# Performance work log

Measured on AMD Instinct MI355X. Metric: run time of the kernel, lower is better.

## Reference

```python
import jax, jax.numpy as jnp
import numpy as np

THRESHOLD = 0.9
EPS = 1e-12


def setup_inputs() -> dict:
    key = jax.random.key(0)
    ks = jax.random.split(key, 7)
    B, D_in, H1, H2, D_out = 8192, 256, 512, 256, 64
    # torch Linear default init ~ U(-1/sqrt(fan_in), 1/sqrt(fan_in)); randn scaled is fine as a stand-in
    def lin(k, out_f, in_f):
        return jax.random.normal(k, (out_f, in_f), dtype=jnp.float32) / np.sqrt(in_f)
    return {
        "x": jax.random.normal(ks[0], (B, D_in), dtype=jnp.float32),
        "W1": lin(ks[1], H1, D_in),
        "b1": jax.random.normal(ks[2], (H1,), dtype=jnp.float32) * 0.01,
        "W2": lin(ks[3], H2, H1),
        "b2": jax.random.normal(ks[4], (H2,), dtype=jnp.float32) * 0.01,
        "W3": lin(ks[5], D_out, H2),
        "b3": jax.random.normal(ks[6], (D_out,), dtype=jnp.float32) * 0.01,
    }


def reference(x, W1, b1, W2, b2, W3, b3):
    # MLP: Linear -> Tanh -> Linear -> Tanh -> Linear (no tanh on last)
    h1 = jnp.tanh(x @ W1.T + b1)          # [B, 512]
    h2 = jnp.tanh(h1 @ W2.T + b2)         # [B, 256]
    out = h2 @ W3.T + b3                  # [B, 64]

    # Pairwise state fidelity: (normalized dot)^2, thresholded adjacency (diag excluded)
    norms = jnp.linalg.norm(out, axis=-1, keepdims=True)  # [B, 1]
    normed = out / (norms + EPS)
    fid = (normed @ normed.T) ** 2                         # [B, B]
    adj = (fid >= THRESHOLD).astype(out.dtype)
    B = out.shape[0]
    adj = adj * (1.0 - jnp.eye(B, dtype=out.dtype))        # no self-edges (i < j pairs only)

    return adj @ out                                       # [B, 64]
```

## Files before the change

### kernel.cpp

```cpp
#include <hip/hip_runtime.h>
#include <hip/hip_bf16.h>
#include <math.h>

#define B_ROWS 8192
#define D_IN   256
#define H1_DIM 512
#define H2_DIM 256
#define D_OUT  64
#define EPSF   1e-12f
#define THRESH 0.9f
#define GUARD 0.94f

typedef __attribute__((ext_vector_type(8))) short short8;
typedef __attribute__((ext_vector_type(4))) float f32x4;

__device__ inline void pack8(const float* __restrict__ src, short* __restrict__ dh,
                             short* __restrict__ dm, int t, int C, int lgq) {
  const int lane = t & 63;
  const int g = t >> 6;
  const int q = g & ((1 << lgq) - 1);
  const int I = g >> lgq;
  const int row = I * 16 + (lane & 15);
  const int k0 = q * 32 + ((lane >> 4) << 3);
  const float* p = src + (size_t)row * C + k0;
  float4 a = *(const float4*)p;
  float4 b = *(const float4*)(p + 4);
  float v[8] = {a.x, a.y, a.z, a.w, b.x, b.y, b.z, b.w};
  short h8[8], m8[8];
#pragma unroll
  for (int e = 0; e < 8; ++e) {
    __hip_bfloat16 h = __float2bfloat16(v[e]);
    float hf = __bfloat162float(h);
    __hip_bfloat16 m = __float2bfloat16(v[e] - hf);
    h8[e] = *(short*)&h;
    m8[e] = *(short*)&m;
  }
  *(short8*)(dh + (size_t)t * 8) = *(short8*)h8;
  *(short8*)(dm + (size_t)t * 8) = *(short8*)m8;
}

__global__ __launch_bounds__(256)
void pack_inputs(const float* __restrict__ x, const float* __restrict__ W1,
                 const float* __restrict__ W2, const float* __restrict__ W3,
                 short* xh, short* xm, short* w1h, short* w1m,
                 short* w2h, short* w2m, short* w3h, short* w3m) {
  const int b = blockIdx.x;
  const int tid = threadIdx.x;
  if (b < 1024)       pack8(x,  xh,  xm,  b * 256 + tid, 256, 3);
  else if (b < 1088)  pack8(W1, w1h, w1m, (b - 1024) * 256 + tid, 256, 3);
  else if (b < 1152)  pack8(W2, w2h, w2m, (b - 1088) * 256 + tid, 512, 4);
  else                pack8(W3, w3h, w3m, (b - 1152) * 256 + tid, 256, 3);
}

template<int KSTEPS, int JT, int MODE>
__global__ __launch_bounds__(256, 2)
void mfma_gemm(const short* __restrict__ pAh, const short* __restrict__ pAm,
               const short* __restrict__ pBh, const short* __restrict__ pBm,
               const float* __restrict__ bias, float* __restrict__ Cout,
               short* __restrict__ dh, short* __restrict__ dm, int N,
               float* __restrict__ rz, float* __restrict__ invng) {
  constexpr int ITB = 4;
  constexpr int BTJ = 2 * JT;
  constexpr int NITEMS = 2 * ITB + 2 * BTJ;
  constexpr int PER_WAVE = NITEMS / 4;
  constexpr int WCOL = 16 * JT + 4;
  union SM {
    struct {
      short Ah[2][ITB * 512];
      short Am[2][ITB * 512];
      short Bh[2][BTJ * 512];
      short Bm[2][BTJ * 512];
    } st;
    float wbuf[4 * 32 * WCOL];
  };
  __shared__ __align__(16) SM sm;
  __shared__ float nsum[2][64];
  __shared__ float invn[64];

  const int tid = threadIdx.x;
  const int wave = tid >> 6, lane = tid & 63;
  const int wi = wave >> 1, wj = wave & 1;
  const int bIt0 = blockIdx.x * ITB;
  const int bJt0 = blockIdx.y * BTJ;

  if constexpr (MODE == 2) {
    float4* rz4 = (float4*)(rz + (size_t)blockIdx.x * 64 * 64);
#pragma unroll
    for (int u = 0; u < 4; ++u)
      rz4[u * 256 + tid] = make_float4(0.f, 0.f, 0.f, 0.f);
  }

  f32x4 acc[2][JT];
#pragma unroll
  for (int a = 0; a < 2; ++a)
#pragma unroll
    for (int b = 0; b < JT; ++b) acc[a][b] = (f32x4){0.f, 0.f, 0.f, 0.f};

  auto stage = [&](int q, int bf) {
#pragma unroll
    for (int u = 0; u < PER_WAVE; ++u) {
      const int item = wave * PER_WAVE + u;
      const short* src;
      short* dst;
      if (item < 2 * ITB) {
        const int t = item >> 1;
        const int m = item & 1;
        src = (m ? pAm : pAh) + ((size_t)(bIt0 + t) * KSTEPS + q) * 512;
        dst = (m ? sm.st.Am : sm.st.Ah)[bf] + t * 512;
      } else {
        const int e = item - 2 * ITB;
        const int t = e >> 1;
        const int m = e & 1;
        src = (m ? pBm : pBh) + ((size_t)(bJt0 + t) * KSTEPS + q) * 512;
        dst = (m ? sm.st.Bm : sm.st.Bh)[bf] + t * 512;
      }
      __builtin_amdgcn_global_load_lds(
          (const __attribute__((address_space(1))) void*)(src + lane * 8),
          (__attribute__((address_space(3))) void*)dst, 16, 0, 0);
    }
  };

  stage(0, 0);
  for (int q = 0; q < KSTEPS; ++q) {
    __syncthreads();
    if (q + 1 < KSTEPS) stage(q + 1, (q + 1) & 1);
    const int bf = q & 1;
    short8 Ah[2], Am[2];
#pragma unroll
    for (int it = 0; it < 2; ++it) {
      Ah[it] = *(const short8*)(sm.st.Ah[bf] + (wi * 2 + it) * 512 + lane * 8);
      Am[it] = *(const short8*)(sm.st.Am[bf] + (wi * 2 + it) * 512 + lane * 8);
    }
    short8 Bh[JT], Bm[JT];
#pragma unroll
    for (int jt = 0; jt < JT; ++jt) {
      Bh[jt] = *(const short8*)(sm.st.Bh[bf] + (wj * JT + jt) * 512 + lane * 8);
      Bm[jt] = *(const short8*)(sm.st.Bm[bf] + (wj * JT + jt) * 512 + lane * 8);
    }
#pragma unroll
    for (int it = 0; it < 2; ++it)
#pragma unroll
      for (int jt = 0; jt < JT; ++jt) {
        acc[it][jt] = __builtin_amdgcn_mfma_f32_16x16x32_bf16(Ah[it], Bh[jt], acc[it][jt], 0, 0, 0);
        acc[it][jt] = __builtin_amdgcn_mfma_f32_16x16x32_bf16(Ah[it], Bm[jt], acc[it][jt], 0, 0, 0);
        acc[it][jt] = __builtin_amdgcn_mfma_f32_16x16x32_bf16(Am[it], Bh[jt], acc[it][jt], 0, 0, 0);
      }
  }
  __syncthreads();

  float bv[JT];
#pragma unroll
  for (int jt = 0; jt < JT; ++jt)
    bv[jt] = bias[(bJt0 + wj * JT + jt) * 16 + (lane & 15)];

  if constexpr (MODE == 1) {
#pragma unroll
    for (int it = 0; it < 2; ++it)
#pragma unroll
      for (int jt = 0; jt < JT; ++jt)
#pragma unroll
        for (int r = 0; r < 4; ++r) {
          const float val = tanhf(acc[it][jt][r] + bv[jt]);
          const int row_l = it * 16 + (lane >> 4) * 4 + r;
          const int col_l = jt * 16 + (lane & 15);
          sm.wbuf[(wave * 32 + row_l) * WCOL + col_l] = val;
        }
    __syncthreads();
  } else {
#pragma unroll
    for (int it = 0; it < 2; ++it)
#pragma unroll
      for (int r = 0; r < 4; ++r) {
        float sq = 0.f;
        const int row_l = it * 16 + (lane >> 4) * 4 + r;
#pragma unroll
        for (int jt = 0; jt < JT; ++jt) {
          const float val = acc[it][jt][r] + bv[jt];
          const int col_l = jt * 16 + (lane & 15);
          sm.wbuf[(wave * 32 + row_l) * WCOL + col_l] = val;
          const int row = (bIt0 + wi * 2 + it) * 16 + (lane >> 4) * 4 + r;
          Cout[(size_t)row * N + wj * (16 * JT) + col_l] = val;
          sq = fmaf(val, val, sq);
        }
#pragma unroll
        for (int m = 1; m < 16; m <<= 1) sq += __shfl_xor(sq, m, 64);
        if ((lane & 15) == 0) nsum[wj][wi * 32 + row_l] = sq;
      }
    __syncthreads();
    if (tid < 64) {
      const float iv = 1.0f / (sqrtf(nsum[0][tid] + nsum[1][tid]) + EPSF);
      invn[tid] = iv;
      invng[blockIdx.x * 64 + tid] = iv;
    }
    __syncthreads();
  }

  constexpr int QLMAX = (JT >= 2) ? (JT / 2) : 1;
#pragma unroll
  for (int itl = 0; itl < 2; ++itl)
#pragma unroll
    for (int ql = 0; ql < QLMAX; ++ql) {
      const int row_l = itl * 16 + (lane & 15);
      const int kl = ql * 32 + ((lane >> 4) << 3);
      const float* wp = &sm.wbuf[(wave * 32 + row_l) * WCOL + kl];
      const float scale = (MODE == 2) ? invn[wi * 32 + row_l] : 1.0f;
      float4 a = *(const float4*)wp;
      float4 b = *(const float4*)(wp + 4);
      float v[8] = {a.x, a.y, a.z, a.w, b.x, b.y, b.z, b.w};
      short h8[8], m8[8];
#pragma unroll
      for (int e = 0; e < 8; ++e) {
        const float sv = v[e] * scale;
        __hip_bfloat16 h = __float2bfloat16(sv);
        h8[e] = *(short*)&h;
        if constexpr (MODE == 1) {
          float hf = __bfloat162float(h);
          __hip_bfloat16 m = __float2bfloat16(sv - hf);
          m8[e] = *(short*)&m;
        }
      }
      const int ItG = bIt0 + wi * 2 + itl;
      const int qG = (((bJt0 + wj * JT) * 16) + ql * 32) >> 5;
      const size_t off = ((size_t)(ItG * (N >> 5) + qG) * 64 + lane) * 8;
      *(short8*)(dh + off) = *(short8*)h8;
      if constexpr (MODE == 1) *(short8*)(dm + off) = *(short8*)m8;
    }
}

#define JSPLIT 8
#define CT 8
#define NCHUNK (B_ROWS / JSPLIT / 16 / CT)

__global__ __launch_bounds__(256, 2)
void gram_accum(const short* __restrict__ vph, const float* __restrict__ out,
                const float* __restrict__ invn, float* __restrict__ res) {
  __shared__ __align__(16) short lh[2][CT * 1024];
  const int tid = threadIdx.x;
  const int wave = tid >> 6;
  const int lane = tid & 63;
  const int i0 = blockIdx.x * 128;
  const int jbase = blockIdx.y * (B_ROWS / JSPLIT);

  short8 Ah[8][2];
#pragma unroll
  for (int it = 0; it < 8; ++it) {
    const int It = (i0 >> 4) + it;
#pragma unroll
    for (int q = 0; q < 2; ++q)
      Ah[it][q] = *(const short8*)(vph + (size_t)It * 1024 + q * 512 + lane * 8);
  }

  auto stage = [&](int c, int bf) {
    const size_t base = ((size_t)(jbase >> 4) + c * CT) * 1024;
#pragma unroll
    for (int u = 0; u < 4; ++u) {
      const int item = wave * 4 + u;
      const short* src = vph + base + item * 512;
      short* dst = lh[bf] + item * 512;
      __builtin_amdgcn_global_load_lds(
          (const __attribute__((address_space(1))) void*)(src + lane * 8),
          (__attribute__((address_space(3))) void*)dst, 16, 0, 0);
    }
  };

  stage(0, 0);
  for (int c = 0; c < NCHUNK; ++c) {
    __syncthreads();
    if (c + 1 < NCHUNK) stage(c + 1, (c + 1) & 1);
    const int bf = c & 1;
#pragma unroll
    for (int t = 0; t < 2; ++t) {
      const int jt = wave * 2 + t;
      const int j0 = jbase + (c * CT + jt) * 16;
      short8 Bh0 = *(const short8*)(lh[bf] + jt * 1024 + lane * 8);
      short8 Bh1 = *(const short8*)(lh[bf] + jt * 1024 + 512 + lane * 8);
      f32x4 g[8];
#pragma unroll
      for (int it = 0; it < 8; ++it) g[it] = (f32x4){0.f, 0.f, 0.f, 0.f};
#pragma unroll
      for (int it = 0; it < 8; ++it) g[it] = __builtin_amdgcn_mfma_f32_16x16x32_bf16(Ah[it][0], Bh0, g[it], 0, 0, 0);
#pragma unroll
      for (int it = 0; it < 8; ++it) g[it] = __builtin_amdgcn_mfma_f32_16x16x32_bf16(Ah[it][1], Bh1, g[it], 0, 0, 0);
#pragma unroll
      for (int it = 0; it < 8; ++it) {
        const float m01 = fmaxf(fabsf(g[it][0]), fabsf(g[it][1]));
        const float m23 = fmaxf(fabsf(g[it][2]), fabsf(g[it][3]));
        if (fmaxf(m01, m23) >= GUARD) {
          const int j = j0 + (lane & 15);
          const float ivj = invn[j];
          const float* __restrict__ oj = out + (size_t)j * D_OUT;
#pragma unroll
          for (int r = 0; r < 4; ++r) {
            if (fabsf(g[it][r]) >= GUARD) {
              const int i = i0 + it * 16 + (lane >> 4) * 4 + r;
              if (i != j) {
                const float* __restrict__ oi = out + (size_t)i * D_OUT;
                float d = 0.f;
                for (int k = 0; k < D_OUT; k += 4) {
                  float4 a = *(const float4*)(oi + k);
                  float4 b = *(const float4*)(oj + k);
                  d = fmaf(a.x, b.x, d); d = fmaf(a.y, b.y, d);
                  d = fmaf(a.z, b.z, d); d = fmaf(a.w, b.w, d);
                }
                const float nd = d * invn[i] * ivj;
                if (nd * nd >= THRESH) {
                  float* __restrict__ ri = res + (size_t)i * D_OUT;
                  for (int k = 0; k < D_OUT; ++k) atomicAdd(&ri[k], oj[k]);
                }
              }
            }
          }
        }
      }
    }
  }
}

#define MB (1024 * 1024)

extern "C" void kernel_launch(void* const* d_in, const int* in_sizes, int n_in,
                              void* d_out, int out_size, void* d_ws, size_t ws_size,
                              hipStream_t stream) {
  const float* x  = (const float*)d_in[0];
  const float* W1 = (const float*)d_in[1];
  const float* b1 = (const float*)d_in[2];
  const float* W2 = (const float*)d_in[3];
  const float* b2 = (const float*)d_in[4];
  const float* W3 = (const float*)d_in[5];
  const float* b3 = (const float*)d_in[6];
  float* res = (float*)d_out;

  char* ws = (char*)d_ws;
  short* xh  = (short*)(ws + 0 * MB);
  short* xm  = (short*)(ws + 4 * MB);
  short* h2h = (short*)(ws + 0 * MB);
  short* h2m = (short*)(ws + 4 * MB);
  short* h1h = (short*)(ws + 8 * MB);
  short* h1m = (short*)(ws + 16 * MB);
  float* out  = (float*)(ws + 8 * MB);
  short* vph  = (short*)(ws + 11 * MB);
  float* invn = (float*)(ws + 12 * MB);
  short* w1h = (short*)(ws + 24 * MB);
  short* w1m = (short*)(ws + 24 * MB + 256 * 1024);
  short* w2h = (short*)(ws + 24 * MB + 512 * 1024);
  short* w2m = (short*)(ws + 24 * MB + 768 * 1024);
  short* w3h = (short*)(ws + 25 * MB);
  short* w3m = (short*)(ws + 25 * MB + 32 * 1024);

  pack_inputs<<<1160, 256, 0, stream>>>(x, W1, W2, W3, xh, xm, w1h, w1m, w2h, w2m, w3h, w3m);
  mfma_gemm<8, 4, 1><<<dim3(128, 4), 256, 0, stream>>>(
      xh, xm, w1h, w1m, b1, nullptr, h1h, h1m, H1_DIM, nullptr, nullptr);
  mfma_gemm<16, 2, 1><<<dim3(128, 4), 256, 0, stream>>>(
      h1h, h1m, w2h, w2m, b2, nullptr, h2h, h2m, H2_DIM, nullptr, nullptr);
  mfma_gemm<8, 2, 2><<<dim3(128, 1), 256, 0, stream>>>(
      h2h, h2m, w3h, w3m, b3, out, vph, nullptr, D_OUT, res, invn);
  gram_accum<<<dim3(B_ROWS / 128, JSPLIT), 256, 0, stream>>>(vph, out, invn, res);
}
```

Before: 127.2 us.

## Fuse three MLP GEMM layers into one kernel keeping activations on-chip

Replaces the x-packing kernel and three separate split-bf16 MFMA GEMM launches with one fused kernel. Each block handles 64 rows, converts x to hi/lo bf16 in registers, and streams W1/W2 chunks through LDS so the h1 and h2 activations never reach global memory. This removes the global round trips for the intermediate activations and two launches. In exchange the grid is only 128 blocks with one block per CU, heavy register use (acc2[16] plus A operands), and many serialized barriers per chunk, so occupancy and latency hiding may suffer.

```diff
diff --git a/kernel.cpp b/kernel.cpp
--- a/kernel.cpp
+++ b/kernel.cpp
@@ -40,191 +40,257 @@
 }
 
 __global__ __launch_bounds__(256)
-void pack_inputs(const float* __restrict__ x, const float* __restrict__ W1,
-                 const float* __restrict__ W2, const float* __restrict__ W3,
-                 short* xh, short* xm, short* w1h, short* w1m,
-                 short* w2h, short* w2m, short* w3h, short* w3m) {
+void pack_weights(const float* __restrict__ W1, const float* __restrict__ W2,
+                  const float* __restrict__ W3,
+                  short* w1h, short* w1m, short* w2h, short* w2m,
+                  short* w3h, short* w3m) {
   const int b = blockIdx.x;
   const int tid = threadIdx.x;
-  if (b < 1024)       pack8(x,  xh,  xm,  b * 256 + tid, 256, 3);
-  else if (b < 1088)  pack8(W1, w1h, w1m, (b - 1024) * 256 + tid, 256, 3);
-  else if (b < 1152)  pack8(W2, w2h, w2m, (b - 1088) * 256 + tid, 512, 4);
-  else                pack8(W3, w3h, w3m, (b - 1152) * 256 + tid, 256, 3);
+  if (b < 64)       pack8(W1, w1h, w1m, b * 256 + tid, 256, 3);
+  else if (b < 128) pack8(W2, w2h, w2m, (b - 64) * 256 + tid, 512, 4);
+  else              pack8(W3, w3h, w3m, (b - 128) * 256 + tid, 256, 3);
 }
 
-template<int KSTEPS, int JT, int MODE>
-__global__ __launch_bounds__(256, 2)
-void mfma_gemm(const short* __restrict__ pAh, const short* __restrict__ pAm,
-               const short* __restrict__ pBh, const short* __restrict__ pBm,
-               const float* __restrict__ bias, float* __restrict__ Cout,
-               short* __restrict__ dh, short* __restrict__ dm, int N,
-               float* __restrict__ rz, float* __restrict__ invng) {
-  constexpr int ITB = 4;
-  constexpr int BTJ = 2 * JT;
-  constexpr int NITEMS = 2 * ITB + 2 * BTJ;
-  constexpr int PER_WAVE = NITEMS / 4;
-  constexpr int WCOL = 16 * JT + 4;
-  union SM {
-    struct {
-      short Ah[2][ITB * 512];
-      short Am[2][ITB * 512];
-      short Bh[2][BTJ * 512];
-      short Bm[2][BTJ * 512];
-    } st;
-    float wbuf[4 * 32 * WCOL];
-  };
-  __shared__ __align__(16) SM sm;
-  __shared__ float nsum[2][64];
-  __shared__ float invn[64];
+__global__ __launch_bounds__(256, 1)
+void fused_mlp(const float* __restrict__ x,
+               const short* __restrict__ w1h, const short* __restrict__ w1m,
+               const short* __restrict__ w2h, const short* __restrict__ w2m,
+               const short* __restrict__ w3h, const short* __restrict__ w3m,
+               const float* __restrict__ b1, const float* __restrict__ b2,
+               const float* __restrict__ b3,
+               float* __restrict__ out, short* __restrict__ vph,
+               float* __restrict__ invng, float* __restrict__ res) {
+  __shared__ __align__(16) short w1s[2 * 2 * 8 * 512];
+  __shared__ __align__(16) short w2s[2 * 16 * 512];
+  __shared__ __align__(16) float tb[4][16][36];
+  __shared__ float invb[64];
 
   const int tid = threadIdx.x;
   const int wave = tid >> 6, lane = tid & 63;
-  const int wi = wave >> 1, wj = wave & 1;
-  const int bIt0 = blockIdx.x * ITB;
-  const int bJt0 = blockIdx.y * BTJ;
-
-  if constexpr (MODE == 2) {
-    float4* rz4 = (float4*)(rz + (size_t)blockIdx.x * 64 * 64);
-#pragma unroll
-    for (int u = 0; u < 4; ++u)
-      rz4[u * 256 + tid] = make_float4(0.f, 0.f, 0.f, 0.f);
-  }
-
-  f32x4 acc[2][JT];
-#pragma unroll
-  for (int a = 0; a < 2; ++a)
-#pragma unroll
-    for (int b = 0; b < JT; ++b) acc[a][b] = (f32x4){0.f, 0.f, 0.f, 0.f};
-
-  auto stage = [&](int q, int bf) {
-#pragma unroll
-    for (int u = 0; u < PER_WAVE; ++u) {
-      const int item = wave * PER_WAVE + u;
-      const short* src;
-      short* dst;
-      if (item < 2 * ITB) {
-        const int t = item >> 1;
-        const int m = item & 1;
-        src = (m ? pAm : pAh) + ((size_t)(bIt0 + t) * KSTEPS + q) * 512;
-        dst = (m ? sm.st.Am : sm.st.Ah)[bf] + t * 512;
-      } else {
-        const int e = item - 2 * ITB;
-        const int t = e >> 1;
-        const int m = e & 1;
-        src = (m ? pBm : pBh) + ((size_t)(bJt0 + t) * KSTEPS + q) * 512;
-        dst = (m ? sm.st.Bm : sm.st.Bh)[bf] + t * 512;
+  const int rr = lane & 15, gg = lane >> 4;
+  const int R0 = blockIdx.x * 64 + wave * 16;
+
+  {
+    float4* rz = (float4*)(res + (size_t)blockIdx.x * 64 * 64);
+#pragma unroll
+    for (int u = 0; u < 4; ++u) rz[u * 256 + tid] = make_float4(0.f, 0.f, 0.f, 0.f);
+  }
+
+  short8 A1h[8], A1m[8];
+#pragma unroll
+  for (int q = 0; q < 8; ++q) {
+    const float* p = x + (size_t)(R0 + rr) * D_IN + q * 32 + gg * 8;
+    float4 a = *(const float4*)p;
+    float4 b = *(const float4*)(p + 4);
+    float v[8] = {a.x, a.y, a.z, a.w, b.x, b.y, b.z, b.w};
+    short h8[8], m8[8];
+#pragma unroll
+    for (int e = 0; e < 8; ++e) {
+      __hip_bfloat16 h = __float2bfloat16(v[e]);
+      float hf = __bfloat162float(h);
+      __hip_bfloat16 m = __float2bfloat16(v[e] - hf);
+      h8[e] = *(short*)&h;
+      m8[e] = *(short*)&m;
+    }
+    A1h[q] = *(short8*)h8;
+    A1m[q] = *(short8*)m8;
+  }
+
+  auto stage_w1 = [&](int c) {
+#pragma unroll
+    for (int u = 0; u < 8; ++u) {
+      const int item = wave * 8 + u;
+      const int m = item >> 4, t = (item >> 3) & 1, q = item & 7;
+      const short* src = (m ? w1m : w1h) + ((size_t)((2 * c + t) * 8 + q)) * 512 + lane * 8;
+      __builtin_amdgcn_global_load_lds(
+          (const __attribute__((address_space(1))) void*)src,
+          (__attribute__((address_space(3))) void*)(w1s + item * 512), 16, 0, 0);
+    }
+  };
+  auto stage_w2 = [&](int c) {
+#pragma unroll
+    for (int u = 0; u < 8; ++u) {
+      const int item = wave * 8 + u;
+      const int m = item >> 4, jt = item & 15;
+      const short* src = (m ? w2m : w2h) + ((size_t)(jt * 16 + c)) * 512 + lane * 8;
+      __builtin_amdgcn_global_load_lds(
+          (const __attribute__((address_space(1))) void*)src,
+          (__attribute__((address_space(3))) void*)(w2s + item * 512), 16, 0, 0);
+    }
+  };
+
+  f32x4 acc2[16];
+#pragma unroll
+  for (int j = 0; j < 16; ++j) acc2[j] = (f32x4){0.f, 0.f, 0.f, 0.f};
+
+  stage_w1(0);
+  stage_w2(0);
+  __syncthreads();
+
+#pragma unroll 1
+  for (int c = 0; c < 16; ++c) {
+    float hv[2][4];
+#pragma unroll
+    for (int jt = 0; jt < 2; ++jt) {
+      f32x4 g = {0.f, 0.f, 0.f, 0.f};
+#pragma unroll
+      for (int q = 0; q < 8; ++q) {
+        short8 Bh = *(const short8*)(w1s + ((jt * 8 + q) << 9) + lane * 8);
+        short8 Bm = *(const short8*)(w1s + (((2 + jt) * 8 + q) << 9) + lane * 8);
+        g = __builtin_amdgcn_mfma_f32_16x16x32_bf16(A1h[q], Bh, g, 0, 0, 0);
+        g = __builtin_amdgcn_mfma_f32_16x16x32_bf16(A1h[q], Bm, g, 0, 0, 0);
+        g = __builtin_amdgcn_mfma_f32_16x16x32_bf16(A1m[q], Bh, g, 0, 0, 0);
       }
-      __builtin_amdgcn_global_load_lds(
-          (const __attribute__((address_space(1))) void*)(src + lane * 8),
-          (__attribute__((address_space(3))) void*)dst, 16, 0, 0);
-    }
-  };
-
-  stage(0, 0);
-  for (int q = 0; q < KSTEPS; ++q) {
-    __syncthreads();
-    if (q + 1 < KSTEPS) stage(q + 1, (q + 1) & 1);
-    const int bf = q & 1;
-    short8 Ah[2], Am[2];
-#pragma unroll
-    for (int it = 0; it < 2; ++it) {
-      Ah[it] = *(const short8*)(sm.st.Ah[bf] + (wi * 2 + it) * 512 + lane * 8);
-      Am[it] = *(const short8*)(sm.st.Am[bf] + (wi * 2 + it) * 512 + lane * 8);
-    }
-    short8 Bh[JT], Bm[JT];
-#pragma unroll
-    for (int jt = 0; jt < JT; ++jt) {
-      Bh[jt] = *(const short8*)(sm.st.Bh[bf] + (wj * JT + jt) * 512 + lane * 8);
-      Bm[jt] = *(const short8*)(sm.st.Bm[bf] + (wj * JT + jt) * 512 + lane * 8);
-    }
-#pragma unroll
-    for (int it = 0; it < 2; ++it)
-#pragma unroll
-      for (int jt = 0; jt < JT; ++jt) {
-        acc[it][jt] = __builtin_amdgcn_mfma_f32_16x16x32_bf16(Ah[it], Bh[jt], acc[it][jt], 0, 0, 0);
-        acc[it][jt] = __builtin_amdgcn_mfma_f32_16x16x32_bf16(Ah[it], Bm[jt], acc[it][jt], 0, 0, 0);
-        acc[it][jt] = __builtin_amdgcn_mfma_f32_16x16x32_bf16(Am[it], Bh[jt], acc[it][jt], 0, 0, 0);
-      }
-  }
-  __syncthreads();
-
-  float bv[JT];
-#pragma unroll
-  for (int jt = 0; jt < JT; ++jt)
-    bv[jt] = bias[(bJt0 + wj * JT + jt) * 16 + (lane & 15)];
-
-  if constexpr (MODE == 1) {
-#pragma unroll
-    for (int it = 0; it < 2; ++it)
-#pragma unroll
-      for (int jt = 0; jt < JT; ++jt)
-#pragma unroll
-        for (int r = 0; r < 4; ++r) {
-          const float val = tanhf(acc[it][jt][r] + bv[jt]);
-          const int row_l = it * 16 + (lane >> 4) * 4 + r;
-          const int col_l = jt * 16 + (lane & 15);
-          sm.wbuf[(wave * 32 + row_l) * WCOL + col_l] = val;
-        }
-    __syncthreads();
-  } else {
-#pragma unroll
-    for (int it = 0; it < 2; ++it)
-#pragma unroll
-      for (int r = 0; r < 4; ++r) {
-        float sq = 0.f;
-        const int row_l = it * 16 + (lane >> 4) * 4 + r;
-#pragma unroll
-        for (int jt = 0; jt < JT; ++jt) {
-          const float val = acc[it][jt][r] + bv[jt];
-          const int col_l = jt * 16 + (lane & 15);
-          sm.wbuf[(wave * 32 + row_l) * WCOL + col_l] = val;
-          const int row = (bIt0 + wi * 2 + it) * 16 + (lane >> 4) * 4 + r;
-          Cout[(size_t)row * N + wj * (16 * JT) + col_l] = val;
-          sq = fmaf(val, val, sq);
-        }
-#pragma unroll
-        for (int m = 1; m < 16; m <<= 1) sq += __shfl_xor(sq, m, 64);
-        if ((lane & 15) == 0) nsum[wj][wi * 32 + row_l] = sq;
-      }
-    __syncthreads();
-    if (tid < 64) {
-      const float iv = 1.0f / (sqrtf(nsum[0][tid] + nsum[1][tid]) + EPSF);
-      invn[tid] = iv;
-      invng[blockIdx.x * 64 + tid] = iv;
-    }
-    __syncthreads();
-  }
-
-  constexpr int QLMAX = (JT >= 2) ? (JT / 2) : 1;
-#pragma unroll
-  for (int itl = 0; itl < 2; ++itl)
-#pragma unroll
-    for (int ql = 0; ql < QLMAX; ++ql) {
-      const int row_l = itl * 16 + (lane & 15);
-      const int kl = ql * 32 + ((lane >> 4) << 3);
-      const float* wp = &sm.wbuf[(wave * 32 + row_l) * WCOL + kl];
-      const float scale = (MODE == 2) ? invn[wi * 32 + row_l] : 1.0f;
-      float4 a = *(const float4*)wp;
-      float4 b = *(const float4*)(wp + 4);
+      const float bv = b1[(2 * c + jt) * 16 + rr];
+#pragma unroll
+      for (int r = 0; r < 4; ++r) hv[jt][r] = tanhf(g[r] + bv);
+    }
+#pragma unroll
+    for (int jt = 0; jt < 2; ++jt)
+#pragma unroll
+      for (int r = 0; r < 4; ++r)
+        tb[wave][gg * 4 + r][jt * 16 + rr] = hv[jt][r];
+    __syncthreads();
+    if (c + 1 < 16) stage_w1(c + 1);
+
+    short8 A2h, A2m;
+    {
+      const float* tp = &tb[wave][rr][gg * 8];
+      float4 a = *(const float4*)tp;
+      float4 b = *(const float4*)(tp + 4);
       float v[8] = {a.x, a.y, a.z, a.w, b.x, b.y, b.z, b.w};
       short h8[8], m8[8];
 #pragma unroll
       for (int e = 0; e < 8; ++e) {
-        const float sv = v[e] * scale;
-        __hip_bfloat16 h = __float2bfloat16(sv);
+        __hip_bfloat16 h = __float2bfloat16(v[e]);
+        float hf = __bfloat162float(h);
+        __hip_bfloat16 m = __float2bfloat16(v[e] - hf);
         h8[e] = *(short*)&h;
-        if constexpr (MODE == 1) {
-          float hf = __bfloat162float(h);
-          __hip_bfloat16 m = __float2bfloat16(sv - hf);
-          m8[e] = *(short*)&m;
-        }
+        m8[e] = *(short*)&m;
       }
-      const int ItG = bIt0 + wi * 2 + itl;
-      const int qG = (((bJt0 + wj * JT) * 16) + ql * 32) >> 5;
-      const size_t off = ((size_t)(ItG * (N >> 5) + qG) * 64 + lane) * 8;
-      *(short8*)(dh + off) = *(short8*)h8;
-      if constexpr (MODE == 1) *(short8*)(dm + off) = *(short8*)m8;
-    }
+      A2h = *(short8*)h8;
+      A2m = *(short8*)m8;
+    }
+#pragma unroll
+    for (int jt2 = 0; jt2 < 16; ++jt2) {
+      short8 Bh = *(const short8*)(w2s + (jt2 << 9) + lane * 8);
+      short8 Bm = *(const short8*)(w2s + ((16 + jt2) << 9) + lane * 8);
+      acc2[jt2] = __builtin_amdgcn_mfma_f32_16x16x32_bf16(A2h, Bh, acc2[jt2], 0, 0, 0);
+      acc2[jt2] = __builtin_amdgcn_mfma_f32_16x16x32_bf16(A2h, Bm, acc2[jt2], 0, 0, 0);
+      acc2[jt2] = __builtin_amdgcn_mfma_f32_16x16x32_bf16(A2m, Bh, acc2[jt2], 0, 0, 0);
+    }
+    __syncthreads();
+    if (c + 1 < 16) stage_w2(c + 1);
+  }
+
+#pragma unroll
+  for (int u = 0; u < 16; ++u) {
+    const int item = wave * 16 + u;
+    const int m = item >> 5, rest = item & 31;
+    const short* src = (m ? w3m : w3h) + ((size_t)rest) * 512 + lane * 8;
+    short* dst = (item < 32) ? (w1s + item * 512) : (w2s + (item - 32) * 512);
+    __builtin_amdgcn_global_load_lds(
+        (const __attribute__((address_space(1))) void*)src,
+        (__attribute__((address_space(3))) void*)dst, 16, 0, 0);
+  }
+
+  short8 A3h[8], A3m[8];
+#pragma unroll
+  for (int q3 = 0; q3 < 8; ++q3) {
+#pragma unroll
+    for (int jt = 0; jt < 2; ++jt) {
+      const int jt2 = q3 * 2 + jt;
+      const float bv = b2[jt2 * 16 + rr];
+#pragma unroll
+      for (int r = 0; r < 4; ++r)
+        tb[wave][gg * 4 + r][jt * 16 + rr] = tanhf(acc2[jt2][r] + bv);
+    }
+    __syncthreads();
+    {
+      const float* tp = &tb[wave][rr][gg * 8];
+      float4 a = *(const float4*)tp;
+      float4 b = *(const float4*)(tp + 4);
+      float v[8] = {a.x, a.y, a.z, a.w, b.x, b.y, b.z, b.w};
+      short h8[8], m8[8];
+#pragma unroll
+      for (int e = 0; e < 8; ++e) {
+        __hip_bfloat16 h = __float2bfloat16(v[e]);
+        float hf = __bfloat162float(h);
+        __hip_bfloat16 m = __float2bfloat16(v[e] - hf);
+        h8[e] = *(short*)&h;
+        m8[e] = *(short*)&m;
+      }
+      A3h[q3] = *(short8*)h8;
+      A3m[q3] = *(short8*)m8;
+    }
+    __syncthreads();
+  }
+
+  f32x4 acc3[4];
+#pragma unroll
+  for (int t = 0; t < 4; ++t) acc3[t] = (f32x4){0.f, 0.f, 0.f, 0.f};
+#pragma unroll
+  for (int q3 = 0; q3 < 8; ++q3)
+#pragma unroll
+    for (int t = 0; t < 4; ++t) {
+      short8 Bh = *(const short8*)(w1s + ((t * 8 + q3) << 9) + lane * 8);
+      short8 Bm = *(const short8*)(w2s + ((t * 8 + q3) << 9) + lane * 8);
+      acc3[t] = __builtin_amdgcn_mfma_f32_16x16x32_bf16(A3h[q3], Bh, acc3[t], 0, 0, 0);
+      acc3[t] = __builtin_amdgcn_mfma_f32_16x16x32_bf16(A3h[q3], Bm, acc3[t], 0, 0, 0);
+      acc3[t] = __builtin_amdgcn_mfma_f32_16x16x32_bf16(A3m[q3], Bh, acc3[t], 0, 0, 0);
+    }
+
+  float val[4][4];
+#pragma unroll
+  for (int t = 0; t < 4; ++t) {
+    const float bv = b3[t * 16 + rr];
+#pragma unroll
+    for (int r = 0; r < 4; ++r) val[t][r] = acc3[t][r] + bv;
+  }
+#pragma unroll
+  for (int t = 0; t < 4; ++t)
+#pragma unroll
+    for (int r = 0; r < 4; ++r)
+      out[(size_t)(R0 + gg * 4 + r) * D_OUT + t * 16 + rr] = val[t][r];
+#pragma unroll
+  for (int r = 0; r < 4; ++r) {
+    float sq = 0.f;
+#pragma unroll
+    for (int t = 0; t < 4; ++t) sq = fmaf(val[t][r], val[t][r], sq);
+#pragma unroll
+    for (int m = 1; m < 16; m <<= 1) sq += __shfl_xor(sq, m, 64);
+    if (rr == 0) {
+      const float iv = 1.0f / (sqrtf(sq) + EPSF);
+      invb[wave * 16 + gg * 4 + r] = iv;
+      invng[R0 + gg * 4 + r] = iv;
+    }
+  }
+  __syncthreads();
+  const int ItG = blockIdx.x * 4 + wave;
+#pragma unroll
+  for (int q = 0; q < 2; ++q) {
+#pragma unroll
+    for (int jt = 0; jt < 2; ++jt)
+#pragma unroll
+      for (int r = 0; r < 4; ++r)
+        tb[wave][gg * 4 + r][jt * 16 + rr] = val[2 * q + jt][r];
+    __syncthreads();
+    {
+      const float* tp = &tb[wave][rr][gg * 8];
+      float4 a = *(const float4*)tp;
+      float4 b = *(const float4*)(tp + 4);
+      const float sc = invb[wave * 16 + rr];
+      float v[8] = {a.x, a.y, a.z, a.w, b.x, b.y, b.z, b.w};
+      short h8[8];
+#pragma unroll
+      for (int e = 0; e < 8; ++e) {
+        __hip_bfloat16 h = __float2bfloat16(v[e] * sc);
+        h8[e] = *(short*)&h;
+      }
+      *(short8*)(vph + ((size_t)(ItG * 2 + q) * 64 + lane) * 8) = *(short8*)h8;
+    }
+    __syncthreads();
+  }
 }
 
 #define JSPLIT 8
@@ -331,12 +397,6 @@
   float* res = (float*)d_out;
 
   char* ws = (char*)d_ws;
-  short* xh  = (short*)(ws + 0 * MB);
-  short* xm  = (short*)(ws + 4 * MB);
-  short* h2h = (short*)(ws + 0 * MB);
-  short* h2m = (short*)(ws + 4 * MB);
-  short* h1h = (short*)(ws + 8 * MB);
-  short* h1m = (short*)(ws + 16 * MB);
   float* out  = (float*)(ws + 8 * MB);
   short* vph  = (short*)(ws + 11 * MB);
   float* invn = (float*)(ws + 12 * MB);
@@ -347,12 +407,8 @@
   short* w3h = (short*)(ws + 25 * MB);
   short* w3m = (short*)(ws + 25 * MB + 32 * 1024);
 
-  pack_inputs<<<1160, 256, 0, stream>>>(x, W1, W2, W3, xh, xm, w1h, w1m, w2h, w2m, w3h, w3m);
-  mfma_gemm<8, 4, 1><<<dim3(128, 4), 256, 0, stream>>>(
-      xh, xm, w1h, w1m, b1, nullptr, h1h, h1m, H1_DIM, nullptr, nullptr);
-  mfma_gemm<16, 2, 1><<<dim3(128, 4), 256, 0, stream>>>(
-      h1h, h1m, w2h, w2m, b2, nullptr, h2h, h2m, H2_DIM, nullptr, nullptr);
-  mfma_gemm<8, 2, 2><<<dim3(128, 1), 256, 0, stream>>>(
-      h2h, h2m, w3h, w3m, b3, out, vph, nullptr, D_OUT, res, invn);
+  pack_weights<<<136, 256, 0, stream>>>(W1, W2, W3, w1h, w1m, w2h, w2m, w3h, w3m);
+  fused_mlp<<<B_ROWS / 64, 256, 0, stream>>>(
+      x, w1h, w1m, w2h, w2m, w3h, w3m, b1, b2, b3, out, vph, invn, res);
   gram_accum<<<dim3(B_ROWS / 128, JSPLIT), 256, 0, stream>>>(vph, out, invn, res);
 }
```

Measured after the change: 145.8 us. +14.7%, slower.

## Fuse fp32-to-bf16 split packing of inputs and weights into GEMM load stages

Applied to the files above, without the earlier changes.

Removes the separate pack_inputs kernel. The GEMMs now load raw fp32 x and weight tiles into registers, split each value into bf16 high and low parts, and write both into shared memory inside the double-buffered K loop. This saves one kernel launch and the write and re-read of the packed buffers. In exchange, weight tiles are re-converted by every block, adding ALU work and register pressure inside the main loop.

```diff
diff --git a/kernel.cpp b/kernel.cpp
--- a/kernel.cpp
+++ b/kernel.cpp
@@ -14,55 +14,18 @@
 typedef __attribute__((ext_vector_type(8))) short short8;
 typedef __attribute__((ext_vector_type(4))) float f32x4;
 
-__device__ inline void pack8(const float* __restrict__ src, short* __restrict__ dh,
-                             short* __restrict__ dm, int t, int C, int lgq) {
-  const int lane = t & 63;
-  const int g = t >> 6;
-  const int q = g & ((1 << lgq) - 1);
-  const int I = g >> lgq;
-  const int row = I * 16 + (lane & 15);
-  const int k0 = q * 32 + ((lane >> 4) << 3);
-  const float* p = src + (size_t)row * C + k0;
-  float4 a = *(const float4*)p;
-  float4 b = *(const float4*)(p + 4);
-  float v[8] = {a.x, a.y, a.z, a.w, b.x, b.y, b.z, b.w};
-  short h8[8], m8[8];
-#pragma unroll
-  for (int e = 0; e < 8; ++e) {
-    __hip_bfloat16 h = __float2bfloat16(v[e]);
-    float hf = __bfloat162float(h);
-    __hip_bfloat16 m = __float2bfloat16(v[e] - hf);
-    h8[e] = *(short*)&h;
-    m8[e] = *(short*)&m;
-  }
-  *(short8*)(dh + (size_t)t * 8) = *(short8*)h8;
-  *(short8*)(dm + (size_t)t * 8) = *(short8*)m8;
-}
-
-__global__ __launch_bounds__(256)
-void pack_inputs(const float* __restrict__ x, const float* __restrict__ W1,
-                 const float* __restrict__ W2, const float* __restrict__ W3,
-                 short* xh, short* xm, short* w1h, short* w1m,
-                 short* w2h, short* w2m, short* w3h, short* w3m) {
-  const int b = blockIdx.x;
-  const int tid = threadIdx.x;
-  if (b < 1024)       pack8(x,  xh,  xm,  b * 256 + tid, 256, 3);
-  else if (b < 1088)  pack8(W1, w1h, w1m, (b - 1024) * 256 + tid, 256, 3);
-  else if (b < 1152)  pack8(W2, w2h, w2m, (b - 1088) * 256 + tid, 512, 4);
-  else                pack8(W3, w3h, w3m, (b - 1152) * 256 + tid, 256, 3);
-}
-
-template<int KSTEPS, int JT, int MODE>
+template<int KSTEPS, int JT, int MODE, bool ARAW>
 __global__ __launch_bounds__(256, 2)
-void mfma_gemm(const short* __restrict__ pAh, const short* __restrict__ pAm,
-               const short* __restrict__ pBh, const short* __restrict__ pBm,
+void mfma_gemm(const float* __restrict__ Araw,
+               const short* __restrict__ pAh, const short* __restrict__ pAm,
+               const float* __restrict__ Braw,
                const float* __restrict__ bias, float* __restrict__ Cout,
                short* __restrict__ dh, short* __restrict__ dm, int N,
                float* __restrict__ rz, float* __restrict__ invng) {
+  constexpr int K = KSTEPS * 32;
   constexpr int ITB = 4;
   constexpr int BTJ = 2 * JT;
-  constexpr int NITEMS = 2 * ITB + 2 * BTJ;
-  constexpr int PER_WAVE = NITEMS / 4;
+  constexpr int BPW = JT / 2;
   constexpr int WCOL = 16 * JT + 4;
   union SM {
     struct {
@@ -75,11 +38,12 @@
   };
   __shared__ __align__(16) SM sm;
   __shared__ float nsum[2][64];
-  __shared__ float invn[64];
+  __shared__ float invb[64];
 
   const int tid = threadIdx.x;
   const int wave = tid >> 6, lane = tid & 63;
   const int wi = wave >> 1, wj = wave & 1;
+  const int rr = lane & 15, gg = lane >> 4;
   const int bIt0 = blockIdx.x * ITB;
   const int bJt0 = blockIdx.y * BTJ;
 
@@ -90,41 +54,76 @@
       rz4[u * 256 + tid] = make_float4(0.f, 0.f, 0.f, 0.f);
   }
 
-  f32x4 acc[2][JT];
-#pragma unroll
-  for (int a = 0; a < 2; ++a)
-#pragma unroll
-    for (int b = 0; b < JT; ++b) acc[a][b] = (f32x4){0.f, 0.f, 0.f, 0.f};
-
-  auto stage = [&](int q, int bf) {
-#pragma unroll
-    for (int u = 0; u < PER_WAVE; ++u) {
-      const int item = wave * PER_WAVE + u;
-      const short* src;
-      short* dst;
-      if (item < 2 * ITB) {
-        const int t = item >> 1;
-        const int m = item & 1;
-        src = (m ? pAm : pAh) + ((size_t)(bIt0 + t) * KSTEPS + q) * 512;
-        dst = (m ? sm.st.Am : sm.st.Ah)[bf] + t * 512;
-      } else {
-        const int e = item - 2 * ITB;
-        const int t = e >> 1;
-        const int m = e & 1;
-        src = (m ? pBm : pBh) + ((size_t)(bJt0 + t) * KSTEPS + q) * 512;
-        dst = (m ? sm.st.Bm : sm.st.Bh)[bf] + t * 512;
-      }
+  float ar[8];
+  float br[BPW][8];
+
+  auto gload8 = [&](const float* __restrict__ p, float* r) {
+    float4 a = *(const float4*)p;
+    float4 b = *(const float4*)(p + 4);
+    r[0] = a.x; r[1] = a.y; r[2] = a.z; r[3] = a.w;
+    r[4] = b.x; r[5] = b.y; r[6] = b.z; r[7] = b.w;
+  };
+
+  auto loads = [&](int q) {
+    if constexpr (ARAW)
+      gload8(Araw + (size_t)((bIt0 + wave) * 16 + rr) * K + q * 32 + gg * 8, ar);
+#pragma unroll
+    for (int u = 0; u < BPW; ++u)
+      gload8(Braw + (size_t)((bJt0 + wave * BPW + u) * 16 + rr) * K + q * 32 + gg * 8, br[u]);
+  };
+
+  auto stageA = [&](int q, int bf) {
+#pragma unroll
+    for (int u = 0; u < 2; ++u) {
+      const int item = wave * 2 + u;
+      const int t = item >> 1, m = item & 1;
+      const short* src = (m ? pAm : pAh) + ((size_t)(bIt0 + t) * KSTEPS + q) * 512;
+      short* dst = (m ? sm.st.Am : sm.st.Ah)[bf] + t * 512;
       __builtin_amdgcn_global_load_lds(
           (const __attribute__((address_space(1))) void*)(src + lane * 8),
           (__attribute__((address_space(3))) void*)dst, 16, 0, 0);
     }
   };
 
-  stage(0, 0);
+  auto split_write = [&](const float* r, short* dsth, short* dstm) {
+    short h8[8], m8[8];
+#pragma unroll
+    for (int e = 0; e < 8; ++e) {
+      __hip_bfloat16 h = __float2bfloat16(r[e]);
+      float hf = __bfloat162float(h);
+      __hip_bfloat16 m = __float2bfloat16(r[e] - hf);
+      h8[e] = *(short*)&h;
+      m8[e] = *(short*)&m;
+    }
+    *(short8*)(dsth + lane * 8) = *(short8*)h8;
+    *(short8*)(dstm + lane * 8) = *(short8*)m8;
+  };
+
+  auto cvt_write = [&](int bf) {
+    if constexpr (ARAW)
+      split_write(ar, sm.st.Ah[bf] + wave * 512, sm.st.Am[bf] + wave * 512);
+#pragma unroll
+    for (int u = 0; u < BPW; ++u)
+      split_write(br[u], sm.st.Bh[bf] + (wave * BPW + u) * 512,
+                         sm.st.Bm[bf] + (wave * BPW + u) * 512);
+  };
+
+  f32x4 acc[2][JT];
+#pragma unroll
+  for (int a = 0; a < 2; ++a)
+#pragma unroll
+    for (int b = 0; b < JT; ++b) acc[a][b] = (f32x4){0.f, 0.f, 0.f, 0.f};
+
+  loads(0);
+  if constexpr (!ARAW) stageA(0, 0);
+  cvt_write(0);
   for (int q = 0; q < KSTEPS; ++q) {
     __syncthreads();
-    if (q + 1 < KSTEPS) stage(q + 1, (q + 1) & 1);
-    const int bf = q & 1;
+    const int bf = q & 1, nbf = (q + 1) & 1;
+    if (q + 1 < KSTEPS) {
+      loads(q + 1);
+      if constexpr (!ARAW) stageA(q + 1, nbf);
+    }
     short8 Ah[2], Am[2];
 #pragma unroll
     for (int it = 0; it < 2; ++it) {
@@ -145,13 +144,14 @@
         acc[it][jt] = __builtin_amdgcn_mfma_f32_16x16x32_bf16(Ah[it], Bm[jt], acc[it][jt], 0, 0, 0);
         acc[it][jt] = __builtin_amdgcn_mfma_f32_16x16x32_bf16(Am[it], Bh[jt], acc[it][jt], 0, 0, 0);
       }
+    if (q + 1 < KSTEPS) cvt_write(nbf);
   }
   __syncthreads();
 
   float bv[JT];
 #pragma unroll
   for (int jt = 0; jt < JT; ++jt)
-    bv[jt] = bias[(bJt0 + wj * JT + jt) * 16 + (lane & 15)];
+    bv[jt] = bias[(bJt0 + wj * JT + jt) * 16 + rr];
 
   if constexpr (MODE == 1) {
 #pragma unroll
@@ -161,8 +161,8 @@
 #pragma unroll
         for (int r = 0; r < 4; ++r) {
           const float val = tanhf(acc[it][jt][r] + bv[jt]);
-          const int row_l = it * 16 + (lane >> 4) * 4 + r;
-          const int col_l = jt * 16 + (lane & 15);
+          const int row_l = it * 16 + gg * 4 + r;
+          const int col_l = jt * 16 + rr;
           sm.wbuf[(wave * 32 + row_l) * WCOL + col_l] = val;
         }
     __syncthreads();
@@ -172,24 +172,24 @@
 #pragma unroll
       for (int r = 0; r < 4; ++r) {
         float sq = 0.f;
-        const int row_l = it * 16 + (lane >> 4) * 4 + r;
+        const int row_l = it * 16 + gg * 4 + r;
 #pragma unroll
         for (int jt = 0; jt < JT; ++jt) {
           const float val = acc[it][jt][r] + bv[jt];
-          const int col_l = jt * 16 + (lane & 15);
+          const int col_l = jt * 16 + rr;
           sm.wbuf[(wave * 32 + row_l) * WCOL + col_l] = val;
-          const int row = (bIt0 + wi * 2 + it) * 16 + (lane >> 4) * 4 + r;
+          const int row = (bIt0 + wi * 2 + it) * 16 + gg * 4 + r;
           Cout[(size_t)row * N + wj * (16 * JT) + col_l] = val;
           sq = fmaf(val, val, sq);
         }
 #pragma unroll
         for (int m = 1; m < 16; m <<= 1) sq += __shfl_xor(sq, m, 64);
-        if ((lane & 15) == 0) nsum[wj][wi * 32 + row_l] = sq;
+        if (rr == 0) nsum[wj][wi * 32 + row_l] = sq;
       }
     __syncthreads();
     if (tid < 64) {
       const float iv = 1.0f / (sqrtf(nsum[0][tid] + nsum[1][tid]) + EPSF);
-      invn[tid] = iv;
+      invb[tid] = iv;
       invng[blockIdx.x * 64 + tid] = iv;
     }
     __syncthreads();
@@ -200,10 +200,10 @@
   for (int itl = 0; itl < 2; ++itl)
 #pragma unroll
     for (int ql = 0; ql < QLMAX; ++ql) {
-      const int row_l = itl * 16 + (lane & 15);
-      const int kl = ql * 32 + ((lane >> 4) << 3);
+      const int row_l = itl * 16 + rr;
+      const int kl = ql * 32 + gg * 8;
       const float* wp = &sm.wbuf[(wave * 32 + row_l) * WCOL + kl];
-      const float scale = (MODE == 2) ? invn[wi * 32 + row_l] : 1.0f;
+      const float scale = (MODE == 2) ? invb[wi * 32 + row_l] : 1.0f;
       float4 a = *(const float4*)wp;
       float4 b = *(const float4*)(wp + 4);
       float v[8] = {a.x, a.y, a.z, a.w, b.x, b.y, b.z, b.w};
@@ -331,8 +331,6 @@
   float* res = (float*)d_out;
 
   char* ws = (char*)d_ws;
-  short* xh  = (short*)(ws + 0 * MB);
-  short* xm  = (short*)(ws + 4 * MB);
   short* h2h = (short*)(ws + 0 * MB);
   short* h2m = (short*)(ws + 4 * MB);
   short* h1h = (short*)(ws + 8 * MB);
@@ -340,19 +338,12 @@
   float* out  = (float*)(ws + 8 * MB);
   short* vph  = (short*)(ws + 11 * MB);
   float* invn = (float*)(ws + 12 * MB);
-  short* w1h = (short*)(ws + 24 * MB);
-  short* w1m = (short*)(ws + 24 * MB + 256 * 1024);
-  short* w2h = (short*)(ws + 24 * MB + 512 * 1024);
-  short* w2m = (short*)(ws + 24 * MB + 768 * 1024);
-  short* w3h = (short*)(ws + 25 * MB);
-  short* w3m = (short*)(ws + 25 * MB + 32 * 1024);
-
-  pack_inputs<<<1160, 256, 0, stream>>>(x, W1, W2, W3, xh, xm, w1h, w1m, w2h, w2m, w3h, w3m);
-  mfma_gemm<8, 4, 1><<<dim3(128, 4), 256, 0, stream>>>(
-      xh, xm, w1h, w1m, b1, nullptr, h1h, h1m, H1_DIM, nullptr, nullptr);
-  mfma_gemm<16, 2, 1><<<dim3(128, 4), 256, 0, stream>>>(
-      h1h, h1m, w2h, w2m, b2, nullptr, h2h, h2m, H2_DIM, nullptr, nullptr);
-  mfma_gemm<8, 2, 2><<<dim3(128, 1), 256, 0, stream>>>(
-      h2h, h2m, w3h, w3m, b3, out, vph, nullptr, D_OUT, res, invn);
+
+  mfma_gemm<8, 4, 1, true><<<dim3(128, 4), 256, 0, stream>>>(
+      x, nullptr, nullptr, W1, b1, nullptr, h1h, h1m, H1_DIM, nullptr, nullptr);
+  mfma_gemm<16, 2, 1, false><<<dim3(128, 4), 256, 0, stream>>>(
+      nullptr, h1h, h1m, W2, b2, nullptr, h2h, h2m, H2_DIM, nullptr, nullptr);
+  mfma_gemm<8, 2, 2, false><<<dim3(128, 1), 256, 0, stream>>>(
+      nullptr, h2h, h2m, W3, b3, out, vph, nullptr, D_OUT, res, invn);
   gram_accum<<<dim3(B_ROWS / 128, JSPLIT), 256, 0, stream>>>(vph, out, invn, res);
 }
```

Result: slower. 139.9 us (+10.0%).

## Fuse x bf16 hi/lo split into first GEMM, holding A fragments in registers

Applied to the files above, without the earlier changes.

The separate packing pass over x is dropped. The first GEMM now loads raw fp32 x tiles into padded shared memory, splits them into bf16 hi/lo fragments, and keeps all K-step A fragments in registers for the whole loop. This removes the write and re-read of the packed x buffers (about 8 MB of traffic) and shrinks the pack kernel to weights only. In exchange it raises register pressure (32 short8 values per thread) and shared-memory use, and each of the 4 column blocks recomputes the split for the same x rows.

```diff
diff --git a/kernel.cpp b/kernel.cpp
--- a/kernel.cpp
+++ b/kernel.cpp
@@ -40,34 +40,36 @@
 }
 
 __global__ __launch_bounds__(256)
-void pack_inputs(const float* __restrict__ x, const float* __restrict__ W1,
-                 const float* __restrict__ W2, const float* __restrict__ W3,
-                 short* xh, short* xm, short* w1h, short* w1m,
-                 short* w2h, short* w2m, short* w3h, short* w3m) {
+void pack_weights(const float* __restrict__ W1, const float* __restrict__ W2,
+                  const float* __restrict__ W3,
+                  short* w1h, short* w1m, short* w2h, short* w2m,
+                  short* w3h, short* w3m) {
   const int b = blockIdx.x;
   const int tid = threadIdx.x;
-  if (b < 1024)       pack8(x,  xh,  xm,  b * 256 + tid, 256, 3);
-  else if (b < 1088)  pack8(W1, w1h, w1m, (b - 1024) * 256 + tid, 256, 3);
-  else if (b < 1152)  pack8(W2, w2h, w2m, (b - 1088) * 256 + tid, 512, 4);
-  else                pack8(W3, w3h, w3m, (b - 1152) * 256 + tid, 256, 3);
+  if (b < 64)       pack8(W1, w1h, w1m, b * 256 + tid, 256, 3);
+  else if (b < 128) pack8(W2, w2h, w2m, (b - 64) * 256 + tid, 512, 4);
+  else              pack8(W3, w3h, w3m, (b - 128) * 256 + tid, 256, 3);
 }
 
-template<int KSTEPS, int JT, int MODE>
+template<int KSTEPS, int JT, int MODE, bool AXREG>
 __global__ __launch_bounds__(256, 2)
-void mfma_gemm(const short* __restrict__ pAh, const short* __restrict__ pAm,
+void mfma_gemm(const float* __restrict__ Araw,
+               const short* __restrict__ pAh, const short* __restrict__ pAm,
                const short* __restrict__ pBh, const short* __restrict__ pBm,
                const float* __restrict__ bias, float* __restrict__ Cout,
                short* __restrict__ dh, short* __restrict__ dm, int N,
                float* __restrict__ rz, float* __restrict__ invng) {
   constexpr int ITB = 4;
   constexpr int BTJ = 2 * JT;
-  constexpr int NITEMS = 2 * ITB + 2 * BTJ;
+  constexpr int NITEMS = (AXREG ? 0 : 2 * ITB) + 2 * BTJ;
   constexpr int PER_WAVE = NITEMS / 4;
   constexpr int WCOL = 16 * JT + 4;
+  constexpr int XP = 257;
   union SM {
+    float xs[AXREG ? 64 * XP : 1];
     struct {
-      short Ah[2][ITB * 512];
-      short Am[2][ITB * 512];
+      short Ah[2][(AXREG ? 1 : ITB) * 512];
+      short Am[2][(AXREG ? 1 : ITB) * 512];
       short Bh[2][BTJ * 512];
       short Bm[2][BTJ * 512];
     } st;
@@ -75,11 +77,12 @@
   };
   __shared__ __align__(16) SM sm;
   __shared__ float nsum[2][64];
-  __shared__ float invn[64];
+  __shared__ float invb[64];
 
   const int tid = threadIdx.x;
   const int wave = tid >> 6, lane = tid & 63;
   const int wi = wave >> 1, wj = wave & 1;
+  const int rr = lane & 15, gg = lane >> 4;
   const int bIt0 = blockIdx.x * ITB;
   const int bJt0 = blockIdx.y * BTJ;
 
@@ -90,11 +93,42 @@
       rz4[u * 256 + tid] = make_float4(0.f, 0.f, 0.f, 0.f);
   }
 
-  f32x4 acc[2][JT];
-#pragma unroll
-  for (int a = 0; a < 2; ++a)
-#pragma unroll
-    for (int b = 0; b < JT; ++b) acc[a][b] = (f32x4){0.f, 0.f, 0.f, 0.f};
+  short8 Axh[AXREG ? 2 : 1][AXREG ? KSTEPS : 1];
+  short8 Axm[AXREG ? 2 : 1][AXREG ? KSTEPS : 1];
+  if constexpr (AXREG) {
+    constexpr int K = KSTEPS * 32;
+#pragma unroll
+    for (int u = 0; u < 16; ++u) {
+      const int f = u * 256 + tid;
+      const int row = f >> 6, c4 = f & 63;
+      *(float4*)&sm.xs[row * XP + c4 * 4] =
+          *(const float4*)(Araw + (size_t)(bIt0 * 16 + row) * K + c4 * 4);
+    }
+    __syncthreads();
+#pragma unroll
+    for (int it = 0; it < 2; ++it) {
+      const int row = (wi * 2 + it) * 16 + rr;
+#pragma unroll
+      for (int q = 0; q < KSTEPS; ++q) {
+        const float* p = &sm.xs[row * XP + q * 32 + gg * 8];
+        float4 a = *(const float4*)p;
+        float4 b = *(const float4*)(p + 4);
+        float v[8] = {a.x, a.y, a.z, a.w, b.x, b.y, b.z, b.w};
+        short h8[8], m8[8];
+#pragma unroll
+        for (int e = 0; e < 8; ++e) {
+          __hip_bfloat16 h = __float2bfloat16(v[e]);
+          float hf = __bfloat162float(h);
+          __hip_bfloat16 m = __float2bfloat16(v[e] - hf);
+          h8[e] = *(short*)&h;
+          m8[e] = *(short*)&m;
+        }
+        Axh[it][q] = *(short8*)h8;
+        Axm[it][q] = *(short8*)m8;
+      }
+    }
+    __syncthreads();
+  }
 
   auto stage = [&](int q, int bf) {
 #pragma unroll
@@ -102,13 +136,13 @@
       const int item = wave * PER_WAVE + u;
       const short* src;
       short* dst;
-      if (item < 2 * ITB) {
+      if (!AXREG && item < 2 * ITB) {
         const int t = item >> 1;
         const int m = item & 1;
         src = (m ? pAm : pAh) + ((size_t)(bIt0 + t) * KSTEPS + q) * 512;
         dst = (m ? sm.st.Am : sm.st.Ah)[bf] + t * 512;
       } else {
-        const int e = item - 2 * ITB;
+        const int e = item - (AXREG ? 0 : 2 * ITB);
         const int t = e >> 1;
         const int m = e & 1;
         src = (m ? pBm : pBh) + ((size_t)(bJt0 + t) * KSTEPS + q) * 512;
@@ -120,7 +154,14 @@
     }
   };
 
+  f32x4 acc[2][JT];
+#pragma unroll
+  for (int a = 0; a < 2; ++a)
+#pragma unroll
+    for (int b = 0; b < JT; ++b) acc[a][b] = (f32x4){0.f, 0.f, 0.f, 0.f};
+
   stage(0, 0);
+#pragma unroll
   for (int q = 0; q < KSTEPS; ++q) {
     __syncthreads();
     if (q + 1 < KSTEPS) stage(q + 1, (q + 1) & 1);
@@ -128,8 +169,13 @@
     short8 Ah[2], Am[2];
 #pragma unroll
     for (int it = 0; it < 2; ++it) {
-      Ah[it] = *(const short8*)(sm.st.Ah[bf] + (wi * 2 + it) * 512 + lane * 8);
-      Am[it] = *(const short8*)(sm.st.Am[bf] + (wi * 2 + it) * 512 + lane * 8);
+      if constexpr (AXREG) {
+        Ah[it] = Axh[it][q];
+        Am[it] = Axm[it][q];
+      } else {
+        Ah[it] = *(const short8*)(sm.st.Ah[bf] + (wi * 2 + it) * 512 + lane * 8);
+        Am[it] = *(const short8*)(sm.st.Am[bf] + (wi * 2 + it) * 512 + lane * 8);
+      }
     }
     short8 Bh[JT], Bm[JT];
 #pragma unroll
@@ -151,7 +197,7 @@
   float bv[JT];
 #pragma unroll
   for (int jt = 0; jt < JT; ++jt)
-    bv[jt] = bias[(bJt0 + wj * JT + jt) * 16 + (lane & 15)];
+    bv[jt] = bias[(bJt0 + wj * JT + jt) * 16 + rr];
 
   if constexpr (MODE == 1) {
 #pragma unroll
@@ -161,8 +207,8 @@
 #pragma unroll
         for (int r = 0; r < 4; ++r) {
           const float val = tanhf(acc[it][jt][r] + bv[jt]);
-          const int row_l = it * 16 + (lane >> 4) * 4 + r;
-          const int col_l = jt * 16 + (lane & 15);
+          const int row_l = it * 16 + gg * 4 + r;
+          const int col_l = jt * 16 + rr;
           sm.wbuf[(wave * 32 + row_l) * WCOL + col_l] = val;
         }
     __syncthreads();
@@ -172,24 +218,24 @@
 #pragma unroll
       for (int r = 0; r < 4; ++r) {
         float sq = 0.f;
-        const int row_l = it * 16 + (lane >> 4) * 4 + r;
+        const int row_l = it * 16 + gg * 4 + r;
 #pragma unroll
         for (int jt = 0; jt < JT; ++jt) {
           const float val = acc[it][jt][r] + bv[jt];
-          const int col_l = jt * 16 + (lane & 15);
+          const int col_l = jt * 16 + rr;
           sm.wbuf[(wave * 32 + row_l) * WCOL + col_l] = val;
-          const int row = (bIt0 + wi * 2 + it) * 16 + (lane >> 4) * 4 + r;
+          const int row = (bIt0 + wi * 2 + it) * 16 + gg * 4 + r;
           Cout[(size_t)row * N + wj * (16 * JT) + col_l] = val;
           sq = fmaf(val, val, sq);
         }
 #pragma unroll
         for (int m = 1; m < 16; m <<= 1) sq += __shfl_xor(sq, m, 64);
-        if ((lane & 15) == 0) nsum[wj][wi * 32 + row_l] = sq;
+        if (rr == 0) nsum[wj][wi * 32 + row_l] = sq;
       }
     __syncthreads();
     if (tid < 64) {
       const float iv = 1.0f / (sqrtf(nsum[0][tid] + nsum[1][tid]) + EPSF);
-      invn[tid] = iv;
+      invb[tid] = iv;
       invng[blockIdx.x * 64 + tid] = iv;
     }
     __syncthreads();
@@ -200,10 +246,10 @@
   for (int itl = 0; itl < 2; ++itl)
 #pragma unroll
     for (int ql = 0; ql < QLMAX; ++ql) {
-      const int row_l = itl * 16 + (lane & 15);
-      const int kl = ql * 32 + ((lane >> 4) << 3);
+      const int row_l = itl * 16 + rr;
+      const int kl = ql * 32 + gg * 8;
       const float* wp = &sm.wbuf[(wave * 32 + row_l) * WCOL + kl];
-      const float scale = (MODE == 2) ? invn[wi * 32 + row_l] : 1.0f;
+      const float scale = (MODE == 2) ? invb[wi * 32 + row_l] : 1.0f;
       float4 a = *(const float4*)wp;
       float4 b = *(const float4*)(wp + 4);
       float v[8] = {a.x, a.y, a.z, a.w, b.x, b.y, b.z, b.w};
@@ -331,8 +377,6 @@
   float* res = (float*)d_out;
 
   char* ws = (char*)d_ws;
-  short* xh  = (short*)(ws + 0 * MB);
-  short* xm  = (short*)(ws + 4 * MB);
   short* h2h = (short*)(ws + 0 * MB);
   short* h2m = (short*)(ws + 4 * MB);
   short* h1h = (short*)(ws + 8 * MB);
@@ -347,12 +391,12 @@
   short* w3h = (short*)(ws + 25 * MB);
   short* w3m = (short*)(ws + 25 * MB + 32 * 1024);
 
-  pack_inputs<<<1160, 256, 0, stream>>>(x, W1, W2, W3, xh, xm, w1h, w1m, w2h, w2m, w3h, w3m);
-  mfma_gemm<8, 4, 1><<<dim3(128, 4), 256, 0, stream>>>(
-      xh, xm, w1h, w1m, b1, nullptr, h1h, h1m, H1_DIM, nullptr, nullptr);
-  mfma_gemm<16, 2, 1><<<dim3(128, 4), 256, 0, stream>>>(
-      h1h, h1m, w2h, w2m, b2, nullptr, h2h, h2m, H2_DIM, nullptr, nullptr);
-  mfma_gemm<8, 2, 2><<<dim3(128, 1), 256, 0, stream>>>(
-      h2h, h2m, w3h, w3m, b3, out, vph, nullptr, D_OUT, res, invn);
+  pack_weights<<<136, 256, 0, stream>>>(W1, W2, W3, w1h, w1m, w2h, w2m, w3h, w3m);
+  mfma_gemm<8, 4, 1, true><<<dim3(128, 4), 256, 0, stream>>>(
+      x, nullptr, nullptr, w1h, w1m, b1, nullptr, h1h, h1m, H1_DIM, nullptr, nullptr);
+  mfma_gemm<16, 2, 1, false><<<dim3(128, 4), 256, 0, stream>>>(
+      nullptr, h1h, h1m, w2h, w2m, b2, nullptr, h2h, h2m, H2_DIM, nullptr, nullptr);
+  mfma_gemm<8, 2, 2, false><<<dim3(128, 1), 256, 0, stream>>>(
+      nullptr, h2h, h2m, w3h, w3m, b3, out, vph, nullptr, D_OUT, res, invn);
   gram_accum<<<dim3(B_ROWS / 128, JSPLIT), 256, 0, stream>>>(vph, out, invn, res);
 }
```

Result: slower. 136.5 us (+7.3%).
